# Performance work log

Measured on AMD Instinct MI355X. Metric: run time of the kernel, lower is better.

The kernel has to match this reference:

```python
import jax, jax.numpy as jnp
import numpy as np

B, S, HIDDEN = 2, 2048, 2048
N_HEADS, N_KV_HEADS = 32, 8
HEAD_DIM = HIDDEN // N_HEADS          # 64
HALF = HEAD_DIM // 2                  # 32
N_REP = N_HEADS // N_KV_HEADS         # 4
NEG_INF = -1e9


def setup_inputs() -> dict:
    key = jax.random.key(0)
    ks = jax.random.split(key, 5)
    scale = 0.02
    x = jax.random.normal(ks[0], (B, S, HIDDEN), dtype=jnp.float32)
    wq = jax.random.normal(ks[1], (HIDDEN, N_HEADS * HEAD_DIM), dtype=jnp.float32) * scale
    wk = jax.random.normal(ks[2], (HIDDEN, N_KV_HEADS * HEAD_DIM), dtype=jnp.float32) * scale
    wv = jax.random.normal(ks[3], (HIDDEN, N_KV_HEADS * HEAD_DIM), dtype=jnp.float32) * scale
    wo = jax.random.normal(ks[4], (HIDDEN, HIDDEN), dtype=jnp.float32) * scale
    # Llama rotary frequencies: theta = 10000^{-2i/d}, angles = pos * theta
    inv_freq = 1.0 / (10000.0 ** (np.arange(0, HEAD_DIM, 2, dtype=np.float32) / HEAD_DIM))
    angles = np.arange(S, dtype=np.float32)[:, None] * inv_freq[None, :]  # [S, HALF]
    freqs_cos = jnp.asarray(np.cos(angles), dtype=jnp.float32)
    freqs_sin = jnp.asarray(np.sin(angles), dtype=jnp.float32)
    mask = jnp.tril(jnp.ones((S, S), dtype=bool))[None, None]  # causal [1,1,S,S]
    return {"x": x, "wq": wq, "wk": wk, "wv": wv, "wo": wo,
            "freqs_cos": freqs_cos, "freqs_sin": freqs_sin, "mask": mask}


def _apply_rope(t, cos, sin):
    # t: [B, S, H, HEAD_DIM]; cos/sin: [S, HALF] -> broadcast [1, S, 1, HALF]
    tr, ti = t[..., ::2], t[..., 1::2]           # real/imag halves (interleaved pairing)
    c = cos[None, :, None, :]
    s = sin[None, :, None, :]
    out_r = tr * c - ti * s
    out_i = tr * s + ti * c
    out = jnp.stack([out_r, out_i], axis=-1)     # [B,S,H,HALF,2]
    return out.reshape(t.shape)                  # re-interleave


def reference(x, wq, wk, wv, wo, freqs_cos, freqs_sin, mask):
    b, s, _ = x.shape
    xq = (x @ wq).reshape(b, s, N_HEADS, HEAD_DIM)
    xk = (x @ wk).reshape(b, s, N_KV_HEADS, HEAD_DIM)
    xv = (x @ wv).reshape(b, s, N_KV_HEADS, HEAD_DIM)
    xq = _apply_rope(xq, freqs_cos, freqs_sin)
    xk = _apply_rope(xk, freqs_cos, freqs_sin)
    # repeat_kv: interleave-repeat kv heads to match query heads
    xk = jnp.repeat(xk, N_REP, axis=2)           # [B,S,N_HEADS,HEAD_DIM]
    xv = jnp.repeat(xv, N_REP, axis=2)
    q = jnp.transpose(xq, (0, 2, 1, 3))          # [B,H,S,D]
    k = jnp.transpose(xk, (0, 2, 1, 3))
    v = jnp.transpose(xv, (0, 2, 1, 3))
    attn = jnp.einsum('bhqd,bhkd->bhqk', q, k) / jnp.sqrt(jnp.float32(HEAD_DIM))
    attn = attn + (1.0 - mask.astype(attn.dtype)) * NEG_INF  # keras Softmax masking
    attn = jax.nn.softmax(attn, axis=-1)
    out = jnp.einsum('bhqk,bhkd->bhqd', attn, v)
    out = jnp.transpose(out, (0, 2, 1, 3)).reshape(b, s, HIDDEN)
    return out @ wo
```

## Files before the change

### kernel.cpp

```cpp
#include <hip/hip_runtime.h>
#include <cstdint>
#include <cstddef>

#define S_LEN 2048
#define HIDDEN 2048
#define NH 32
#define NKV 8
#define HD 64
#define QKV_W 3072

typedef __bf16 bf16;
typedef __bf16 bf16x8 __attribute__((ext_vector_type(8)));
typedef __bf16 bf16x4 __attribute__((ext_vector_type(4)));
typedef float f32x4 __attribute__((ext_vector_type(4)));

__device__ __forceinline__ void async16(const bf16* g, bf16* l) {
  __builtin_amdgcn_global_load_lds((const __attribute__((address_space(1))) void*)g,
                                   (__attribute__((address_space(3))) void*)l, 16, 0, 0);
}

__device__ __forceinline__ int swz8(int row, int col) {
  return (((col >> 3) ^ (row & 7)) << 3) | (col & 7);
}

__global__ void cast_x_kernel(const float* __restrict__ in, bf16* __restrict__ out, int n4) {
  int i = blockIdx.x * blockDim.x + threadIdx.x;
  if (i >= n4) return;
  f32x4 v = ((const f32x4*)in)[i];
  bf16x4 o;
  o[0] = (bf16)v[0]; o[1] = (bf16)v[1]; o[2] = (bf16)v[2]; o[3] = (bf16)v[3];
  ((bf16x4*)out)[i] = o;
}

__global__ void transpose_cast_kernel(const float* __restrict__ in, bf16* __restrict__ out,
                                      int K, int N) {
  __shared__ float tile[32][33];
  const int n0 = blockIdx.x * 32, k0 = blockIdx.y * 32;
  const int tx = threadIdx.x, ty = threadIdx.y;
#pragma unroll
  for (int i = 0; i < 32; i += 8)
    tile[ty + i][tx] = in[(size_t)(k0 + ty + i) * N + n0 + tx];
  __syncthreads();
#pragma unroll
  for (int i = 0; i < 32; i += 8)
    out[(size_t)(n0 + ty + i) * K + k0 + tx] = (bf16)tile[tx][ty + i];
}

__global__ void vt_kernel(const bf16* __restrict__ qkv, bf16* __restrict__ vt) {
  __shared__ bf16 tile[32][33];
  const int s0 = blockIdx.x * 32, c0 = blockIdx.y * 32, b = blockIdx.z;
  const int tx = threadIdx.x, ty = threadIdx.y;
#pragma unroll
  for (int i = 0; i < 32; i += 8)
    tile[ty + i][tx] = qkv[((size_t)b * S_LEN + s0 + ty + i) * QKV_W + 2560 + c0 + tx];
  __syncthreads();
#pragma unroll
  for (int i = 0; i < 32; i += 8)
    vt[((size_t)b * 512 + c0 + ty + i) * S_LEN + s0 + tx] = tile[tx][ty + i];
}

template <int OUT_BF16>
__global__ __launch_bounds__(256) void gemm_bt_kernel(const bf16* __restrict__ A,
                                                      const bf16* __restrict__ Bt,
                                                      void* __restrict__ Cv,
                                                      int M, int N, int K) {
  __shared__ bf16 Al[128 * 32];
  __shared__ bf16 Bl[128 * 32];
  const int tid = threadIdx.x;
  const int lane = tid & 63, w = tid >> 6;
  const int quad = lane >> 4, l16 = lane & 15;
  const int m0 = blockIdx.y * 128, n0 = blockIdx.x * 128;
  const int wm = (w >> 1) * 64, wn = (w & 1) * 64;
  f32x4 acc[4][4] = {};
  const int srow = tid >> 2, scol = (tid & 3) * 8;
  const bf16* Ar0 = A + (size_t)(m0 + srow) * K + scol;
  const bf16* Ar1 = A + (size_t)(m0 + 64 + srow) * K + scol;
  const bf16* Br0 = Bt + (size_t)(n0 + srow) * K + scol;
  const bf16* Br1 = Bt + (size_t)(n0 + 64 + srow) * K + scol;
  bf16* al0 = Al + tid * 8;
  bf16* al1 = Al + 2048 + tid * 8;
  bf16* bl0 = Bl + tid * 8;
  bf16* bl1 = Bl + 2048 + tid * 8;
  for (int kt = 0; kt < K; kt += 32) {
    __syncthreads();
    async16(Ar0 + kt, al0);
    async16(Ar1 + kt, al1);
    async16(Br0 + kt, bl0);
    async16(Br1 + kt, bl1);
    __syncthreads();
    bf16x8 a[4], b[4];
#pragma unroll
    for (int mi = 0; mi < 4; ++mi)
      a[mi] = *(const bf16x8*)(Al + (wm + mi * 16 + l16) * 32 + quad * 8);
#pragma unroll
    for (int ni = 0; ni < 4; ++ni)
      b[ni] = *(const bf16x8*)(Bl + (wn + ni * 16 + l16) * 32 + quad * 8);
#pragma unroll
    for (int mi = 0; mi < 4; ++mi)
#pragma unroll
      for (int ni = 0; ni < 4; ++ni)
        acc[mi][ni] = __builtin_amdgcn_mfma_f32_16x16x32_bf16(a[mi], b[ni], acc[mi][ni], 0, 0, 0);
  }
#pragma unroll
  for (int mi = 0; mi < 4; ++mi)
#pragma unroll
    for (int ni = 0; ni < 4; ++ni)
#pragma unroll
      for (int i = 0; i < 4; ++i) {
        const int row = m0 + wm + mi * 16 + quad * 4 + i;
        const int col = n0 + wn + ni * 16 + l16;
        if (OUT_BF16)
          ((bf16*)Cv)[(size_t)row * N + col] = (bf16)acc[mi][ni][i];
        else
          ((float*)Cv)[(size_t)row * N + col] = acc[mi][ni][i];
      }
}

__global__ void rope_kernel(bf16* __restrict__ qkv, const float* __restrict__ cosp,
                            const float* __restrict__ sinp, int total) {
  int idx = blockIdx.x * blockDim.x + threadIdx.x;
  if (idx >= total) return;
  const int row = idx / 320;
  const int col = (idx - row * 320) * 8;
  const int s = row & (S_LEN - 1);
  const int j0 = (col >> 1) & 31;
  bf16* ptr = qkv + (size_t)row * QKV_W + col;
  bf16x8 v = *(bf16x8*)ptr;
#pragma unroll
  for (int u = 0; u < 4; ++u) {
    const float tr = (float)v[2 * u], ti = (float)v[2 * u + 1];
    const float c = cosp[s * 32 + j0 + u], sn = sinp[s * 32 + j0 + u];
    v[2 * u] = (bf16)(tr * c - ti * sn);
    v[2 * u + 1] = (bf16)(tr * sn + ti * c);
  }
  *(bf16x8*)ptr = v;
}

__global__ __launch_bounds__(256) void attn_kernel(const bf16* __restrict__ qkv,
                                                   const bf16* __restrict__ vt,
                                                   bf16* __restrict__ out) {
  __shared__ bf16 Kl[2][64 * 64];
  __shared__ bf16 Vl[2][64 * 64];
  __shared__ bf16 Pl[4][32 * 64];
  const int tid = threadIdx.x;
  const int lane = tid & 63, w = tid >> 6;
  const int quad = lane >> 4, l16 = lane & 15;
  int id = blockIdx.x;
  const int kvh = id & 7; id >>= 3;
  const int gx = id & 7; id >>= 3;
  const int rep = id & 3; const int b = id >> 2;
  const int h = kvh * 4 + rep;
  const bf16* Qbase = qkv + ((size_t)b * S_LEN) * QKV_W + h * HD;
  const bf16* Kbase = qkv + ((size_t)b * S_LEN) * QKV_W + 2048 + kvh * HD;
  const bf16* Vtb = vt + ((size_t)b * 512 + kvh * 64) * S_LEN;
  const int srow = tid >> 3;
  const int gcol = ((tid & 7) ^ (srow & 7)) * 8;
  const bf16* Ksrc0 = Kbase + (size_t)srow * QKV_W + gcol;
  const bf16* Ksrc1 = Kbase + (size_t)(srow + 32) * QKV_W + gcol;
  const bf16* Vsrc0 = Vtb + (size_t)srow * S_LEN + gcol;
  const bf16* Vsrc1 = Vtb + (size_t)(srow + 32) * S_LEN + gcol;

  for (int pass = 0; pass < 2; ++pass) {
    const int qt = pass ? (15 - gx) : gx;
    const int qbase = qt * 128 + w * 32;
    bf16x8 aq[2][2];
#pragma unroll
    for (int g = 0; g < 2; ++g) {
      const size_t qr = (size_t)(qbase + g * 16 + l16) * QKV_W;
      aq[g][0] = *(const bf16x8*)(Qbase + qr + quad * 8);
      aq[g][1] = *(const bf16x8*)(Qbase + qr + 32 + quad * 8);
    }
    float lsum0 = 0.f, lsum1 = 0.f;
    f32x4 o[2][4] = {};

    const int nt = 2 * qt + 2;
    async16(Ksrc0, &Kl[0][tid * 8]);
    async16(Ksrc1, &Kl[0][2048 + tid * 8]);
    async16(Vsrc0, &Vl[0][tid * 8]);
    async16(Vsrc1, &Vl[0][2048 + tid * 8]);
    __syncthreads();

    for (int t = 0; t < nt; ++t) {
      const int cur = t & 1;
      if (t + 1 < nt) {
        const int kn = (t + 1) * 64;
        async16(Ksrc0 + (size_t)kn * QKV_W, &Kl[cur ^ 1][tid * 8]);
        async16(Ksrc1 + (size_t)kn * QKV_W, &Kl[cur ^ 1][2048 + tid * 8]);
        async16(Vsrc0 + kn, &Vl[cur ^ 1][tid * 8]);
        async16(Vsrc1 + kn, &Vl[cur ^ 1][2048 + tid * 8]);
      }
      const int kt = t * 64;
      const bool on0 = kt <= qbase + 15;
      const bool on1 = kt <= qbase + 31;
      if (on1) {
        f32x4 c[2][4] = {};
#pragma unroll
        for (int j = 0; j < 4; ++j) {
          const int kr = j * 16 + l16;
          const bf16x8 bk0 = *(const bf16x8*)&Kl[cur][kr * 64 + swz8(kr, quad * 8)];
          const bf16x8 bk1 = *(const bf16x8*)&Kl[cur][kr * 64 + swz8(kr, 32 + quad * 8)];
          c[1][j] = __builtin_amdgcn_mfma_f32_16x16x32_bf16(bk0, aq[1][0], c[1][j], 0, 0, 0);
          c[1][j] = __builtin_amdgcn_mfma_f32_16x16x32_bf16(bk1, aq[1][1], c[1][j], 0, 0, 0);
          if (on0) {
            c[0][j] = __builtin_amdgcn_mfma_f32_16x16x32_bf16(bk0, aq[0][0], c[0][j], 0, 0, 0);
            c[0][j] = __builtin_amdgcn_mfma_f32_16x16x32_bf16(bk1, aq[0][1], c[0][j], 0, 0, 0);
          }
        }
#pragma unroll
        for (int g = 0; g < 2; ++g) {
          if (!(g ? on1 : on0)) continue;
          const int qrow = qbase + g * 16;
          float p[4][4];
#pragma unroll
          for (int j = 0; j < 4; ++j)
#pragma unroll
            for (int i = 0; i < 4; ++i)
              p[j][i] = exp2f(fmaf(c[g][j][i], 0.18033688f, -5.7707801f));
          if (kt + 63 > qrow) {
            const int qabs = qrow + l16;
#pragma unroll
            for (int j = 0; j < 4; ++j)
#pragma unroll
              for (int i = 0; i < 4; ++i)
                if (kt + j * 16 + quad * 4 + i > qabs) p[j][i] = 0.f;
          }
          float ls = 0.f;
#pragma unroll
          for (int j = 0; j < 4; ++j) {
            ls += (p[j][0] + p[j][1]) + (p[j][2] + p[j][3]);
            bf16x4 pv;
            pv[0] = (bf16)p[j][0]; pv[1] = (bf16)p[j][1];
            pv[2] = (bf16)p[j][2]; pv[3] = (bf16)p[j][3];
            const int pr = g * 16 + l16;
            *(bf16x4*)&Pl[w][pr * 64 + swz8(pr, j * 16 + quad * 4)] = pv;
          }
          if (g) lsum1 += ls; else lsum0 += ls;
        }
        bf16x8 ap0l, ap0h, ap1l, ap1h;
        {
          const int pr1 = 16 + l16;
          ap1l = *(const bf16x8*)&Pl[w][pr1 * 64 + swz8(pr1, quad * 8)];
          ap1h = *(const bf16x8*)&Pl[w][pr1 * 64 + swz8(pr1, 32 + quad * 8)];
          if (on0) {
            ap0l = *(const bf16x8*)&Pl[w][l16 * 64 + swz8(l16, quad * 8)];
            ap0h = *(const bf16x8*)&Pl[w][l16 * 64 + swz8(l16, 32 + quad * 8)];
          }
        }
#pragma unroll
        for (int dt = 0; dt < 4; ++dt) {
          const int vr = dt * 16 + l16;
          const bf16x8 bv0 = *(const bf16x8*)&Vl[cur][vr * 64 + swz8(vr, quad * 8)];
          const bf16x8 bv1 = *(const bf16x8*)&Vl[cur][vr * 64 + swz8(vr, 32 + quad * 8)];
          o[1][dt] = __builtin_amdgcn_mfma_f32_16x16x32_bf16(ap1l, bv0, o[1][dt], 0, 0, 0);
          o[1][dt] = __builtin_amdgcn_mfma_f32_16x16x32_bf16(ap1h, bv1, o[1][dt], 0, 0, 0);
          if (on0) {
            o[0][dt] = __builtin_amdgcn_mfma_f32_16x16x32_bf16(ap0l, bv0, o[0][dt], 0, 0, 0);
            o[0][dt] = __builtin_amdgcn_mfma_f32_16x16x32_bf16(ap0h, bv1, o[0][dt], 0, 0, 0);
          }
        }
      }
      __syncthreads();
    }
#pragma unroll
    for (int g = 0; g < 2; ++g) {
      float ls = g ? lsum1 : lsum0;
      ls += __shfl_xor(ls, 16);
      ls += __shfl_xor(ls, 32);
      const float rlq = 1.0f / ls;
#pragma unroll
      for (int i = 0; i < 4; ++i) {
        const float rl = __shfl(rlq, (lane & 48) | (quad * 4 + i));
        const int r = qbase + g * 16 + quad * 4 + i;
#pragma unroll
        for (int dt = 0; dt < 4; ++dt)
          out[((size_t)b * S_LEN + r) * HIDDEN + h * HD + dt * 16 + l16] =
              (bf16)(o[g][dt][i] * rl);
      }
    }
  }
}

extern "C" void kernel_launch(void* const* d_in, const int* in_sizes, int n_in,
                              void* d_out, int out_size, void* d_ws, size_t ws_size,
                              hipStream_t stream) {
  const float* x = (const float*)d_in[0];
  const float* wq = (const float*)d_in[1];
  const float* wk = (const float*)d_in[2];
  const float* wv = (const float*)d_in[3];
  const float* wo = (const float*)d_in[4];
  const float* fc = (const float*)d_in[5];
  const float* fs = (const float*)d_in[6];

  char* ws = (char*)d_ws;
  bf16* xb   = (bf16*)(ws);
  bf16* wT   = (bf16*)(ws + 16777216);
  bf16* woT  = (bf16*)(ws + 29360128);
  bf16* qkv  = (bf16*)(ws + 37748736);
  bf16* aout = (bf16*)(ws + 62914560);
  bf16* vt   = xb;

  cast_x_kernel<<<8192, 256, 0, stream>>>(x, xb, 2097152);
  transpose_cast_kernel<<<dim3(64, 64), dim3(32, 8), 0, stream>>>(wq, wT, 2048, 2048);
  transpose_cast_kernel<<<dim3(16, 64), dim3(32, 8), 0, stream>>>(wk, wT + (size_t)2048 * 2048, 2048, 512);
  transpose_cast_kernel<<<dim3(16, 64), dim3(32, 8), 0, stream>>>(wv, wT + (size_t)2560 * 2048, 2048, 512);
  transpose_cast_kernel<<<dim3(64, 64), dim3(32, 8), 0, stream>>>(wo, woT, 2048, 2048);

  gemm_bt_kernel<1><<<dim3(24, 32), 256, 0, stream>>>(xb, wT, (void*)qkv, 4096, 3072, 2048);
  rope_kernel<<<5120, 256, 0, stream>>>(qkv, fc, fs, 1310720);
  vt_kernel<<<dim3(64, 16, 2), dim3(32, 8), 0, stream>>>(qkv, vt);
  attn_kernel<<<512, 256, 0, stream>>>(qkv, vt, aout);
  gemm_bt_kernel<0><<<dim3(16, 32), 256, 0, stream>>>(aout, woT, d_out, 4096, 2048, 2048);
}
```

Measured before the change: 349.8 us.

## Use 256x256 tiled 8-wave GEMM with interleaved async loads for QKV projection

Adds a new GEMM kernel with 256x256 block tiles, 512 threads, double-buffered async global-to-LDS loads split into K-halves, and priority raising around MFMA bursts. The QKV projection now uses it instead of the 128x128 GEMM. The goal is more operand reuse per block and overlap of loads with matrix math. The trade-off is a grid of only 192 blocks, which may underfill the GPU's compute units.

```diff
diff --git a/kernel.cpp b/kernel.cpp
--- a/kernel.cpp
+++ b/kernel.cpp
@@ -116,6 +116,133 @@
       }
 }
 
+template <int OUT_BF16>
+__global__ __launch_bounds__(512, 2) void gemm256_kernel(const bf16* __restrict__ A,
+                                                         const bf16* __restrict__ Bt,
+                                                         void* __restrict__ Cv,
+                                                         int M, int N, int K) {
+  __shared__ bf16 AL[2][2][256 * 32];
+  __shared__ bf16 BL[2][2][256 * 32];
+  const int tid = threadIdx.x;
+  const int lane = tid & 63;
+  const int quad = lane >> 4, l16 = lane & 15;
+  const int w = tid >> 6;
+  const int wr = w >> 2, wc = w & 3;
+  const int m0 = blockIdx.y * 256, n0 = blockIdx.x * 256;
+  const int r0 = tid >> 2, g0 = tid & 3;
+  const bf16* Abase = A + (size_t)m0 * K;
+  const bf16* Bbase = Bt + (size_t)n0 * K;
+  const int swg0 = (g0 ^ (r0 & 3)) * 8;
+
+  int aoff[8], boff[4];
+#pragma unroll
+  for (int mf = 0; mf < 8; ++mf) {
+    const int row = wr * 128 + mf * 16 + l16;
+    aoff[mf] = row * 32 + ((quad ^ (row & 3)) * 8);
+  }
+#pragma unroll
+  for (int nf = 0; nf < 4; ++nf) {
+    const int row = wc * 64 + nf * 16 + l16;
+    boff[nf] = row * 32 + ((quad ^ (row & 3)) * 8);
+  }
+
+#define STAGE_HALF(dst, base, koff)                                                  \
+  do {                                                                               \
+    async16((base) + (size_t)r0 * K + (koff) + swg0, (dst) + tid * 8);               \
+    async16((base) + (size_t)(r0 + 128) * K + (koff) + swg0, (dst) + 4096 + tid * 8);\
+  } while (0)
+
+  const int NT = K >> 6;
+  STAGE_HALF(AL[0][0], Abase, 0);
+  STAGE_HALF(BL[0][0], Bbase, 0);
+  STAGE_HALF(AL[0][1], Abase, 32);
+  STAGE_HALF(BL[0][1], Bbase, 32);
+  asm volatile("s_waitcnt vmcnt(4)" ::: "memory");
+  __builtin_amdgcn_sched_barrier(0);
+  __builtin_amdgcn_s_barrier();
+  __builtin_amdgcn_sched_barrier(0);
+
+  f32x4 acc[8][4] = {};
+  for (int t = 0; t < NT; ++t) {
+    const int buf = t & 1, nbuf = buf ^ 1;
+    const int tn = (t + 1 < NT) ? t + 1 : t;
+    const int kn = tn * 64;
+    bf16x8 a[8], b0, b1;
+#pragma unroll
+    for (int mf = 0; mf < 8; ++mf) a[mf] = *(const bf16x8*)&AL[buf][0][aoff[mf]];
+    b0 = *(const bf16x8*)&BL[buf][0][boff[0]];
+    b1 = *(const bf16x8*)&BL[buf][0][boff[1]];
+    STAGE_HALF(AL[nbuf][0], Abase, kn);
+    __builtin_amdgcn_s_barrier();
+    __builtin_amdgcn_sched_barrier(0);
+    __builtin_amdgcn_s_setprio(1);
+#pragma unroll
+    for (int mf = 0; mf < 8; ++mf) {
+      acc[mf][0] = __builtin_amdgcn_mfma_f32_16x16x32_bf16(a[mf], b0, acc[mf][0], 0, 0, 0);
+      acc[mf][1] = __builtin_amdgcn_mfma_f32_16x16x32_bf16(a[mf], b1, acc[mf][1], 0, 0, 0);
+    }
+    __builtin_amdgcn_s_setprio(0);
+    b0 = *(const bf16x8*)&BL[buf][0][boff[2]];
+    b1 = *(const bf16x8*)&BL[buf][0][boff[3]];
+    STAGE_HALF(BL[nbuf][0], Bbase, kn);
+    asm volatile("s_waitcnt vmcnt(4)" ::: "memory");
+    __builtin_amdgcn_sched_barrier(0);
+    __builtin_amdgcn_s_barrier();
+    __builtin_amdgcn_sched_barrier(0);
+    __builtin_amdgcn_s_setprio(1);
+#pragma unroll
+    for (int mf = 0; mf < 8; ++mf) {
+      acc[mf][2] = __builtin_amdgcn_mfma_f32_16x16x32_bf16(a[mf], b0, acc[mf][2], 0, 0, 0);
+      acc[mf][3] = __builtin_amdgcn_mfma_f32_16x16x32_bf16(a[mf], b1, acc[mf][3], 0, 0, 0);
+    }
+    __builtin_amdgcn_s_setprio(0);
+#pragma unroll
+    for (int mf = 0; mf < 8; ++mf) a[mf] = *(const bf16x8*)&AL[buf][1][aoff[mf]];
+    b0 = *(const bf16x8*)&BL[buf][1][boff[0]];
+    b1 = *(const bf16x8*)&BL[buf][1][boff[1]];
+    STAGE_HALF(AL[nbuf][1], Abase, kn + 32);
+    __builtin_amdgcn_s_barrier();
+    __builtin_amdgcn_sched_barrier(0);
+    __builtin_amdgcn_s_setprio(1);
+#pragma unroll
+    for (int mf = 0; mf < 8; ++mf) {
+      acc[mf][0] = __builtin_amdgcn_mfma_f32_16x16x32_bf16(a[mf], b0, acc[mf][0], 0, 0, 0);
+      acc[mf][1] = __builtin_amdgcn_mfma_f32_16x16x32_bf16(a[mf], b1, acc[mf][1], 0, 0, 0);
+    }
+    __builtin_amdgcn_s_setprio(0);
+    b0 = *(const bf16x8*)&BL[buf][1][boff[2]];
+    b1 = *(const bf16x8*)&BL[buf][1][boff[3]];
+    STAGE_HALF(BL[nbuf][1], Bbase, kn + 32);
+    asm volatile("s_waitcnt vmcnt(4)" ::: "memory");
+    __builtin_amdgcn_sched_barrier(0);
+    __builtin_amdgcn_s_barrier();
+    __builtin_amdgcn_sched_barrier(0);
+    __builtin_amdgcn_s_setprio(1);
+#pragma unroll
+    for (int mf = 0; mf < 8; ++mf) {
+      acc[mf][2] = __builtin_amdgcn_mfma_f32_16x16x32_bf16(a[mf], b0, acc[mf][2], 0, 0, 0);
+      acc[mf][3] = __builtin_amdgcn_mfma_f32_16x16x32_bf16(a[mf], b1, acc[mf][3], 0, 0, 0);
+    }
+    __builtin_amdgcn_s_setprio(0);
+  }
+#undef STAGE_HALF
+  asm volatile("s_waitcnt vmcnt(0)" ::: "memory");
+  __builtin_amdgcn_s_barrier();
+#pragma unroll
+  for (int mf = 0; mf < 8; ++mf)
+#pragma unroll
+    for (int nf = 0; nf < 4; ++nf)
+#pragma unroll
+      for (int i = 0; i < 4; ++i) {
+        const int row = m0 + wr * 128 + mf * 16 + quad * 4 + i;
+        const int col = n0 + wc * 64 + nf * 16 + l16;
+        if (OUT_BF16)
+          ((bf16*)Cv)[(size_t)row * N + col] = (bf16)acc[mf][nf][i];
+        else
+          ((float*)Cv)[(size_t)row * N + col] = acc[mf][nf][i];
+      }
+}
+
 __global__ void rope_kernel(bf16* __restrict__ qkv, const float* __restrict__ cosp,
                             const float* __restrict__ sinp, int total) {
   int idx = blockIdx.x * blockDim.x + threadIdx.x;
@@ -305,7 +432,7 @@
   transpose_cast_kernel<<<dim3(16, 64), dim3(32, 8), 0, stream>>>(wv, wT + (size_t)2560 * 2048, 2048, 512);
   transpose_cast_kernel<<<dim3(64, 64), dim3(32, 8), 0, stream>>>(wo, woT, 2048, 2048);
 
-  gemm_bt_kernel<1><<<dim3(24, 32), 256, 0, stream>>>(xb, wT, (void*)qkv, 4096, 3072, 2048);
+  gemm256_kernel<1><<<dim3(12, 16), 512, 0, stream>>>(xb, wT, (void*)qkv, 4096, 3072, 2048);
   rope_kernel<<<5120, 256, 0, stream>>>(qkv, fc, fs, 1310720);
   vt_kernel<<<dim3(64, 16, 2), dim3(32, 8), 0, stream>>>(qkv, vt);
   attn_kernel<<<512, 256, 0, stream>>>(qkv, vt, aout);
```

After: 335.7 us. 4.0% less time.
